# Optimization experiments

Measured on AMD Instinct MI355X. Metric: run time of the kernel, lower is better.

Reference implementation:

```python
import jax, jax.numpy as jnp
import numpy as np

B, S, D = 2, 4096, 1024
H, HD = 16, 64
CF = 0.5
K = int(S * CF)          # top_k tokens routed through the block
HIDDEN = 4 * D
EPS = 1e-5
SCALE = 1.0 / float(np.sqrt(HD))


def rmsnorm(x, w):
    return x * jax.lax.rsqrt(jnp.mean(x * x, axis=-1, keepdims=True) + EPS) * w


def rope(x, cos, sin):
    # x: [B,K,H,HD]; cos/sin: [K, HD//2]
    x1, x2 = x[..., ::2], x[..., 1::2]
    c = cos[None, :, None, :]
    s = sin[None, :, None, :]
    r1 = x1 * c - x2 * s
    r2 = x1 * s + x2 * c
    return jnp.stack([r1, r2], axis=-1).reshape(x.shape)


def block(x, mask, cos, sin, attn_norm, wq, wk, wv, wo, ffn_norm, w1, w2, w3):
    # Llama-style decoder block on the routed subset x: [B,K,D]
    b, k, _ = x.shape
    xn = rmsnorm(x, attn_norm)
    q = (xn @ wq).reshape(b, k, H, HD)
    kk = (xn @ wk).reshape(b, k, H, HD)
    v = (xn @ wv).reshape(b, k, H, HD)
    q = rope(q, cos, sin)
    kk = rope(kk, cos, sin)
    scores = jnp.einsum('bqhd,bkhd->bhqk', q, kk) * SCALE
    scores = jnp.where(mask[None, None], scores, jnp.finfo(scores.dtype).min)
    attn = jax.nn.softmax(scores, axis=-1)
    o = jnp.einsum('bhqk,bkhd->bqhd', attn, v).reshape(b, k, D)
    h = x + o @ wo
    hn = rmsnorm(h, ffn_norm)
    return h + (jax.nn.silu(hn @ w1) * (hn @ w3)) @ w2


def setup_inputs() -> dict:
    key = jax.random.key(0)
    ks = jax.random.split(key, 10)
    sc = 0.02
    inv = 1.0 / (10000.0 ** (np.arange(0, HD, 2, dtype=np.float32) / HD))
    ang = np.outer(np.arange(K, dtype=np.float32), inv)  # [K, HD//2]
    return {
        'x': jax.random.normal(ks[0], (B, S, D), jnp.float32),
        'mask': jnp.tril(jnp.ones((K, K), dtype=bool)),
        'freqs_cos': jnp.asarray(np.cos(ang)),
        'freqs_sin': jnp.asarray(np.sin(ang)),
        'w_router': jax.random.normal(ks[1], (D, 1), jnp.float32) * sc,
        'attn_norm': jnp.ones((D,), jnp.float32),
        'wq': jax.random.normal(ks[2], (D, D), jnp.float32) * sc,
        'wk': jax.random.normal(ks[3], (D, D), jnp.float32) * sc,
        'wv': jax.random.normal(ks[4], (D, D), jnp.float32) * sc,
        'wo': jax.random.normal(ks[5], (D, D), jnp.float32) * sc,
        'ffn_norm': jnp.ones((D,), jnp.float32),
        'w1': jax.random.normal(ks[6], (D, HIDDEN), jnp.float32) * sc,
        'w2': jax.random.normal(ks[7], (HIDDEN, D), jnp.float32) * sc,
        'w3': jax.random.normal(ks[8], (D, HIDDEN), jnp.float32) * sc,
    }


def reference(x, mask, freqs_cos, freqs_sin, w_router, attn_norm, wq, wk, wv, wo, ffn_norm, w1, w2, w3):
    b = x.shape[0]
    router_logits = (x @ w_router)[..., 0]            # [B,S]
    vals, idx = jax.lax.top_k(router_logits, K)       # [B,K]
    order = jnp.argsort(idx, axis=1)                  # torch.sort of token_index
    sel = jnp.take_along_axis(idx, order, axis=1)     # sorted selected positions
    token_w = jax.nn.softmax(vals, axis=1)            # softmax over topk weights
    r_weights = jnp.take_along_axis(token_w, order, axis=1)  # [B,K]
    filtered_x = jnp.take_along_axis(x, sel[:, :, None], axis=1)  # [B,K,D]
    x_out = block(filtered_x, mask, freqs_cos, freqs_sin, attn_norm,
                  wq, wk, wv, wo, ffn_norm, w1, w2, w3)
    xw_out = r_weights[:, :, None] * x_out
    # scatter_add back into the residual stream
    out = x.at[jnp.arange(b)[:, None], sel, :].add(xw_out)
    return out
```

## Files before the change

### kernel.cpp

```cpp
#include <hip/hip_runtime.h>
#include <cstdint>
#include <cstddef>

typedef unsigned short u16;
typedef __bf16 bf16x8 __attribute__((ext_vector_type(8)));
typedef short s16x4 __attribute__((ext_vector_type(4)));
typedef float f32x4 __attribute__((ext_vector_type(4)));

#define SCALE_Q_LOG2E 0.18033688011112042f

static __device__ __forceinline__ float b2f(u16 u){ return __uint_as_float(((unsigned)u)<<16); }
static __device__ __forceinline__ u16 f2b(float f){
  unsigned u = __float_as_uint(f);
  return (u16)((u + 0x7fffu + ((u>>16)&1u)) >> 16);
}
static __device__ __forceinline__ void gload_lds16(const void* g, void* l){
  auto gp = reinterpret_cast<__attribute__((address_space(1))) uint32_t*>(reinterpret_cast<uintptr_t>(g));
  auto lp = reinterpret_cast<__attribute__((address_space(3))) uint32_t*>(reinterpret_cast<uintptr_t>(l));
  __builtin_amdgcn_global_load_lds(gp, lp, 16, 0, 0);
}
static __device__ __forceinline__ f32x4 mfma16bf(s16x4 a, s16x4 b, f32x4 c){
#if __has_builtin(__builtin_amdgcn_mfma_f32_16x16x16bf16_1k)
  return __builtin_amdgcn_mfma_f32_16x16x16bf16_1k(a, b, c, 0, 0, 0);
#else
  f32x4 d = c;
  asm volatile("v_mfma_f32_16x16x16_bf16 %0, %1, %2, %0" : "+v"(d) : "v"(a), "v"(b));
  return d;
#endif
}

__global__ __launch_bounds__(256) void prep_kernel(
    const float* __restrict__ wq, const float* __restrict__ wk,
    const float* __restrict__ wv, const float* __restrict__ wo,
    const float* __restrict__ w1, const float* __restrict__ w3,
    const float* __restrict__ w2, const float* __restrict__ x,
    const float* __restrict__ wr,
    u16* __restrict__ WqkvT, u16* __restrict__ WoT,
    u16* __restrict__ W13T, u16* __restrict__ W2T,
    float* __restrict__ logits, float* __restrict__ out){
  __shared__ float tile[32][33];
  int bx = blockIdx.x;
  if (bx < 12288 || (bx >= 12288 && bx < 13312) || (bx>=13312 && bx<16384)){ }
  if (bx < 16384){
    const float* in; u16* outp; int R, C, rowmap, tcol, trow;
    if (bx < 4096){
      int wsel = bx>>10, tid = bx&1023;
      in = (wsel==0)?wq:(wsel==1)?wk:(wsel==2)?wv:wo;
      outp = (wsel<3) ? (WqkvT + (size_t)wsel*1024*1024) : WoT;
      R=1024; C=1024; rowmap=0; tcol=tid&31; trow=tid>>5;
    } else if (bx < 12288){
      int wsel=(bx-4096)>>12, tid=(bx-4096)&4095;
      in = wsel ? w3 : w1; outp = W13T; R=1024; C=4096; rowmap=1+wsel;
      tcol=tid&127; trow=tid>>7;
    } else {
      int tid = bx-12288;
      in = w2; outp = W2T; R=4096; C=1024; rowmap=0;
      tcol=tid&31; trow=tid>>5;
    }
    int t=threadIdx.x, tx=t&31, ty=t>>5;
    int c0=tcol*32, r0=trow*32;
    #pragma unroll
    for (int i=0;i<4;i++) tile[ty+i*8][tx] = in[(size_t)(r0+ty+i*8)*C + c0+tx];
    __syncthreads();
    #pragma unroll
    for (int i=0;i<4;i++){
      int c = c0+ty+i*8;
      int orow = c;
      if (rowmap==1) orow = (c>>4)*32 + (c&15);
      else if (rowmap==2) orow = (c>>4)*32 + 16 + (c&15);
      outp[(size_t)orow*R + r0+tx] = f2b(tile[tx][ty+i*8]);
    }
  } else if (bx < 18432){
    int row = (bx-16384)*4 + (threadIdx.x>>6);
    int l = threadIdx.x & 63;
    const float4* xr = (const float4*)(x + (size_t)row*1024) + l;
    const float4* wp = (const float4*)wr + l;
    float acc = 0.f;
    #pragma unroll
    for (int c=0;c<4;c++){
      float4 xv = xr[c*64];
      float4 wv = wp[c*64];
      acc += xv.x*wv.x + xv.y*wv.y + xv.z*wv.z + xv.w*wv.w;
    }
    #pragma unroll
    for (int m=1;m<64;m<<=1) acc += __shfl_xor(acc, m, 64);
    if (l==0) logits[row] = acc;
  } else {
    size_t idx = ((size_t)(bx-18432)*256 + threadIdx.x)*4;
    *(float4*)(out+idx) = *(const float4*)(x+idx);
  }
}

__global__ __launch_bounds__(256) void transpose_bf16(const u16* __restrict__ in, u16* __restrict__ out,
                                                      int R, int C){
  __shared__ u16 tile[32][33];
  size_t zoff = (size_t)blockIdx.z * R * C;
  const u16* ip = in + zoff;
  u16* op = out + zoff;
  int tx = threadIdx.x, ty = threadIdx.y;
  int c0 = blockIdx.x*32, r0 = blockIdx.y*32;
  #pragma unroll
  for (int i=0;i<4;i++) tile[ty+i*8][tx] = ip[(size_t)(r0+ty+i*8)*C + c0+tx];
  __syncthreads();
  #pragma unroll
  for (int i=0;i<4;i++) op[(size_t)(c0+ty+i*8)*R + r0+tx] = tile[tx][ty+i*8];
}

static __device__ __forceinline__ unsigned mapkey(float f){
  unsigned u = __float_as_uint(f);
  return (u & 0x80000000u) ? ~u : (u | 0x80000000u);
}
static __device__ unsigned blk_scan_excl(unsigned cnt, unsigned* swav){
  int t = threadIdx.x; int l = t&63, w = t>>6;
  unsigned v = cnt;
  #pragma unroll
  for (int off=1; off<64; off<<=1){
    unsigned n = __shfl_up(v, off, 64);
    if (l >= off) v += n;
  }
  __syncthreads();
  if (l==63) swav[w] = v;
  __syncthreads();
  if (t==0){ unsigned c=0; for (int i=0;i<16;i++){ unsigned tmp=swav[i]; swav[i]=c; c+=tmp; } }
  __syncthreads();
  return swav[w] + v - cnt;
}
__global__ __launch_bounds__(1024) void topk_kernel(const float* __restrict__ logits,
        int* __restrict__ sel, float* __restrict__ rw, int* __restrict__ inv){
  int b = blockIdx.x, t = threadIdx.x;
  int l = t&63, w = t>>6;
  __shared__ float vals[4096];
  __shared__ unsigned hist[256];
  __shared__ unsigned swav[16];
  __shared__ float fwav[16];
  __shared__ unsigned sh_prefix, sh_remaining;
  const float* lgp = logits + b*4096;
  for (int i=t;i<4096;i+=1024) vals[i]=lgp[i];
  if (t==0){ sh_prefix=0u; sh_remaining=2048u; }
  __syncthreads();
  for (int level=0; level<4; level++){
    int shift = 24 - level*8;
    if (t<256) hist[t]=0u;
    __syncthreads();
    unsigned pfx = sh_prefix;
    for (int i=t;i<4096;i+=1024){
      unsigned key = mapkey(vals[i]);
      if (level==0 || (key >> (shift+8)) == pfx)
        atomicAdd(&hist[(key>>shift)&255u], 1u);
    }
    __syncthreads();
    if (t==0){
      unsigned rem = sh_remaining, cum=0u; unsigned bsel=0u;
      for (int bin=255; bin>=0; bin--){
        unsigned hc = hist[bin];
        if (cum + hc >= rem){ bsel=(unsigned)bin; break; }
        cum += hc;
      }
      sh_remaining = rem - cum;
      sh_prefix = (pfx<<8) | bsel;
    }
    __syncthreads();
  }
  unsigned T = sh_prefix;
  unsigned req = sh_remaining;
  int i0 = t*4;
  unsigned gt_[4], eq_[4], fl_[4]; float v_[4];
  #pragma unroll
  for (int j=0;j<4;j++){
    v_[j] = vals[i0+j];
    unsigned key = mapkey(v_[j]);
    gt_[j] = key > T ? 1u:0u;
    eq_[j] = key == T ? 1u:0u;
  }
  unsigned eqbase = blk_scan_excl(eq_[0]+eq_[1]+eq_[2]+eq_[3], swav);
  unsigned er = eqbase;
  #pragma unroll
  for (int j=0;j<4;j++){ fl_[j] = gt_[j] | (eq_[j] & (er < req ? 1u:0u)); er += eq_[j]; }
  unsigned pbase = blk_scan_excl(fl_[0]+fl_[1]+fl_[2]+fl_[3], swav);
  unsigned p = pbase;
  #pragma unroll
  for (int j=0;j<4;j++){
    int i = i0+j;
    if (fl_[j]){ sel[b*2048+(int)p]=i; inv[b*4096+i]=(int)p; p++; }
    else inv[b*4096+i] = -1;
  }
  float mx = fmaxf(fmaxf(v_[0],v_[1]), fmaxf(v_[2],v_[3]));
  #pragma unroll
  for (int m=1;m<64;m<<=1) mx = fmaxf(mx, __shfl_xor(mx,m,64));
  __syncthreads();
  if (l==0) fwav[w]=mx;
  __syncthreads();
  if (t==0){ float g=fwav[0]; for(int i=1;i<16;i++) g=fmaxf(g,fwav[i]); fwav[0]=g; }
  __syncthreads();
  float gm = fwav[0];
  float zz = 0.f;
  #pragma unroll
  for (int j=0;j<4;j++) if (fl_[j]) zz += expf(v_[j]-gm);
  #pragma unroll
  for (int m=1;m<64;m<<=1) zz += __shfl_xor(zz,m,64);
  __syncthreads();
  if (l==0) fwav[w]=zz;
  __syncthreads();
  if (t==0){ float s=0.f; for(int i=0;i<16;i++) s+=fwav[i]; fwav[0]=s; }
  __syncthreads();
  float Z = fwav[0];
  unsigned p2 = pbase;
  #pragma unroll
  for (int j=0;j<4;j++) if (fl_[j]){ rw[b*2048+(int)p2] = expf(v_[j]-gm)/Z; p2++; }
}

__global__ __launch_bounds__(256) void rmsnorm_kernel(const float* __restrict__ xin,
        const float* __restrict__ gamma, const int* __restrict__ sel,
        u16* __restrict__ xn){
  int r = blockIdx.x;
  int src = r;
  if (sel) src = (r>>11)*4096 + sel[r];
  const float* row = xin + (size_t)src*1024;
  int t = threadIdx.x, l = t&63, w = t>>6;
  int d0 = t*4;
  float4 xv = *(const float4*)(row + d0);
  float ss = xv.x*xv.x + xv.y*xv.y + xv.z*xv.z + xv.w*xv.w;
  #pragma unroll
  for (int m=1;m<64;m<<=1) ss += __shfl_xor(ss,m,64);
  __shared__ float red[4];
  if (l==0) red[w]=ss;
  __syncthreads();
  float tot = red[0]+red[1]+red[2]+red[3];
  float rms = rsqrtf(tot*(1.f/1024.f) + 1e-5f);
  float4 gv = *(const float4*)(gamma + d0);
  u16 o0=f2b(xv.x*rms*gv.x), o1=f2b(xv.y*rms*gv.y), o2=f2b(xv.z*rms*gv.z), o3=f2b(xv.w*rms*gv.w);
  uint2 ov; ov.x = (unsigned)o0 | ((unsigned)o1<<16); ov.y = (unsigned)o2 | ((unsigned)o3<<16);
  *(uint2*)(xn + (size_t)r*1024 + d0) = ov;
}

template<int BK>
static __device__ __forceinline__ int swz(int row, int blk){
  if constexpr (BK==64) return blk ^ (row&7);
  else                  return blk ^ ((row>>1)&3);
}

template<int BN, int BK, typename OT>
__global__ __launch_bounds__(256,2) void gemm_bt(const u16* __restrict__ A, const u16* __restrict__ Bt,
        OT* __restrict__ C, const float* __restrict__ resid, const int* __restrict__ sel,
        int M, int N, int Kd){
  __shared__ u16 As[128*BK];
  __shared__ u16 Bs[BN*BK];
  constexpr int NF = BN/32;
  constexpr int KK = BK/32;
  int t = threadIdx.x, w = t>>6, l = t&63, lg = l>>4, ln = l&15;
  int m0 = blockIdx.y*128, n0 = blockIdx.x*BN;
  int wm = (w&1)*64, wn = (w>>1)*(BN/2);
  f32x4 acc[4][NF] = {};
  for (int k0=0; k0<Kd; k0+=BK){
    __syncthreads();
    #pragma unroll
    for (int c=0;c<128*BK*2/4096;c++){
      int off = t*16 + c*4096;
      int row = off/(BK*2), pb = (off%(BK*2))>>4;
      gload_lds16(A + (size_t)(m0+row)*Kd + k0 + swz<BK>(row,pb)*8, &As[c*2048 + w*512]);
    }
    #pragma unroll
    for (int c=0;c<BN*BK*2/4096;c++){
      int off = t*16 + c*4096;
      int row = off/(BK*2), pb = (off%(BK*2))>>4;
      gload_lds16(Bt + (size_t)(n0+row)*Kd + k0 + swz<BK>(row,pb)*8, &Bs[c*2048 + w*512]);
    }
    __syncthreads();
    #pragma unroll
    for (int kk=0;kk<KK;kk++){
      bf16x8 af[4], bfv[NF];
      #pragma unroll
      for (int i=0;i<4;i++){
        int r = wm+i*16+ln;
        af[i] = *(const bf16x8*)&As[r*BK + swz<BK>(r, kk*4+lg)*8];
      }
      #pragma unroll
      for (int i=0;i<NF;i++){
        int r = wn+i*16+ln;
        bfv[i] = *(const bf16x8*)&Bs[r*BK + swz<BK>(r, kk*4+lg)*8];
      }
      #pragma unroll
      for (int mi=0;mi<4;mi++)
        #pragma unroll
        for (int ni=0;ni<NF;ni++)
          acc[mi][ni] = __builtin_amdgcn_mfma_f32_16x16x32_bf16(af[mi], bfv[ni], acc[mi][ni], 0,0,0);
    }
  }
  #pragma unroll
  for (int mi=0;mi<4;mi++){
    #pragma unroll
    for (int ni=0;ni<NF;ni++){
      #pragma unroll
      for (int r=0;r<4;r++){
        int row = m0+wm+mi*16+lg*4+r;
        int col = n0+wn+ni*16+ln;
        float v = acc[mi][ni][r];
        if (resid){
          size_t rrow = sel ? ((size_t)(row>>11)*4096 + sel[row]) : (size_t)row;
          v += resid[rrow*N + col];
        }
        if constexpr (sizeof(OT)==2) C[(size_t)row*N + col] = f2b(v);
        else                          C[(size_t)row*N + col] = v;
      }
    }
  }
}

__global__ __launch_bounds__(256,2) void gemm_w2(const u16* __restrict__ A, const u16* __restrict__ Bt,
        const float* __restrict__ x, const float* __restrict__ hbuf,
        const int* __restrict__ sel, const float* __restrict__ rw,
        float* __restrict__ out, int Kd){
  constexpr int BN = 64, BK = 64;
  __shared__ u16 As[128*BK];
  __shared__ u16 Bs[BN*BK];
  int t = threadIdx.x, w = t>>6, l = t&63, lg = l>>4, ln = l&15;
  int m0 = blockIdx.y*128, n0 = blockIdx.x*BN;
  int wm = (w&1)*64, wn = (w>>1)*(BN/2);
  f32x4 acc[4][2] = {};
  for (int k0=0; k0<Kd; k0+=BK){
    __syncthreads();
    #pragma unroll
    for (int c=0;c<4;c++){
      int off = t*16 + c*4096;
      int row = off/(BK*2), pb = (off%(BK*2))>>4;
      gload_lds16(A + (size_t)(m0+row)*Kd + k0 + swz<BK>(row,pb)*8, &As[c*2048 + w*512]);
    }
    #pragma unroll
    for (int c=0;c<2;c++){
      int off = t*16 + c*4096;
      int row = off/(BK*2), pb = (off%(BK*2))>>4;
      gload_lds16(Bt + (size_t)(n0+row)*Kd + k0 + swz<BK>(row,pb)*8, &Bs[c*2048 + w*512]);
    }
    __syncthreads();
    #pragma unroll
    for (int kk=0;kk<2;kk++){
      bf16x8 af[4], bfv[2];
      #pragma unroll
      for (int i=0;i<4;i++){
        int r = wm+i*16+ln;
        af[i] = *(const bf16x8*)&As[r*BK + swz<BK>(r, kk*4+lg)*8];
      }
      #pragma unroll
      for (int i=0;i<2;i++){
        int r = wn+i*16+ln;
        bfv[i] = *(const bf16x8*)&Bs[r*BK + swz<BK>(r, kk*4+lg)*8];
      }
      #pragma unroll
      for (int mi=0;mi<4;mi++)
        #pragma unroll
        for (int ni=0;ni<2;ni++)
          acc[mi][ni] = __builtin_amdgcn_mfma_f32_16x16x32_bf16(af[mi], bfv[ni], acc[mi][ni], 0,0,0);
    }
  }
  #pragma unroll
  for (int mi=0;mi<4;mi++){
    int row0 = m0+wm+mi*16+lg*4;
    #pragma unroll
    for (int r=0;r<4;r++){
      int row = row0+r;
      int b = row>>11;
      size_t srow = (size_t)b*4096 + sel[row];
      float wgt = rw[row];
      #pragma unroll
      for (int ni=0;ni<2;ni++){
        int col = n0+wn+ni*16+ln;
        float y = acc[mi][ni][r];
        float v = x[srow*1024 + col] + wgt*(hbuf[(size_t)row*1024 + col] + y);
        out[srow*1024 + col] = v;
      }
    }
  }
}

__global__ __launch_bounds__(256,2) void gemm13(const u16* __restrict__ A, const u16* __restrict__ Bt,
        u16* __restrict__ g, int Kd){
  constexpr int BK = 64;
  __shared__ u16 As[128*BK];
  __shared__ u16 Bs[128*BK];
  int t = threadIdx.x, w = t>>6, l = t&63, lg = l>>4, ln = l&15;
  int m0 = blockIdx.y*128, n0 = blockIdx.x*128;
  int wm = (w&1)*64, wn = (w>>1)*64;
  f32x4 acc[4][4] = {};
  for (int k0=0; k0<Kd; k0+=BK){
    __syncthreads();
    #pragma unroll
    for (int c=0;c<4;c++){
      int off = t*16 + c*4096;
      int row = off/(BK*2), pb = (off%(BK*2))>>4;
      gload_lds16(A  + (size_t)(m0+row)*Kd + k0 + swz<BK>(row,pb)*8, &As[c*2048 + w*512]);
      gload_lds16(Bt + (size_t)(n0+row)*Kd + k0 + swz<BK>(row,pb)*8, &Bs[c*2048 + w*512]);
    }
    __syncthreads();
    #pragma unroll
    for (int kk=0;kk<2;kk++){
      bf16x8 af[4], bfv[4];
      #pragma unroll
      for (int i=0;i<4;i++){
        int ra = wm+i*16+ln, rb = wn+i*16+ln;
        af[i]  = *(const bf16x8*)&As[ra*BK + swz<BK>(ra, kk*4+lg)*8];
        bfv[i] = *(const bf16x8*)&Bs[rb*BK + swz<BK>(rb, kk*4+lg)*8];
      }
      #pragma unroll
      for (int mi=0;mi<4;mi++)
        #pragma unroll
        for (int ni=0;ni<4;ni++)
          acc[mi][ni] = __builtin_amdgcn_mfma_f32_16x16x32_bf16(af[mi], bfv[ni], acc[mi][ni], 0,0,0);
    }
  }
  int gbase = (n0+wn)>>1;
  #pragma unroll
  for (int mi=0;mi<4;mi++){
    #pragma unroll
    for (int p=0;p<2;p++){
      #pragma unroll
      for (int r=0;r<4;r++){
        int row = m0+wm+mi*16+lg*4+r;
        int col = gbase + p*16 + ln;
        float a1 = acc[mi][2*p][r], a3 = acc[mi][2*p+1][r];
        float s1 = a1 / (1.f + __expf(-a1));
        g[(size_t)row*4096 + col] = f2b(s1*a3);
      }
    }
  }
}

__global__ __launch_bounds__(256) void rope_kernel(const u16* __restrict__ QKV,
        const float* __restrict__ fcos, const float* __restrict__ fsin,
        u16* __restrict__ q_r, u16* __restrict__ k_r, u16* __restrict__ v_r){
  int row = blockIdx.x;
  int tok = row & 2047;
  int t = threadIdx.x;
  int d0 = t*4;
  int h = d0 >> 6, wd = d0 & 63, i0 = wd >> 1;
  const u16* base = QKV + (size_t)row*3072;
  size_t ob = (((size_t)(row>>11)*16 + h)*2048 + (size_t)tok)*64 + wd;
  float c0 = fcos[tok*32+i0],   s0 = fsin[tok*32+i0];
  float c1 = fcos[tok*32+i0+1], s1 = fsin[tok*32+i0+1];
  const u16* qp = base + d0;
  float x0=b2f(qp[0]), x1=b2f(qp[1]), x2=b2f(qp[2]), x3=b2f(qp[3]);
  q_r[ob]   = f2b((x0*c0-x1*s0)*SCALE_Q_LOG2E);
  q_r[ob+1] = f2b((x0*s0+x1*c0)*SCALE_Q_LOG2E);
  q_r[ob+2] = f2b((x2*c1-x3*s1)*SCALE_Q_LOG2E);
  q_r[ob+3] = f2b((x2*s1+x3*c1)*SCALE_Q_LOG2E);
  const u16* kp = base + 1024 + d0;
  x0=b2f(kp[0]); x1=b2f(kp[1]); x2=b2f(kp[2]); x3=b2f(kp[3]);
  k_r[ob]   = f2b(x0*c0-x1*s0);
  k_r[ob+1] = f2b(x0*s0+x1*c0);
  k_r[ob+2] = f2b(x2*c1-x3*s1);
  k_r[ob+3] = f2b(x2*s1+x3*c1);
  const u16* vp = base + 2048 + d0;
  v_r[ob]=vp[0]; v_r[ob+1]=vp[1]; v_r[ob+2]=vp[2]; v_r[ob+3]=vp[3];
}

static __device__ __forceinline__ void flash_tile(
    const bf16x8 (&kf)[4][2], const s16x4 (&vf)[4][4],
    bf16x8 qf0, bf16x8 qf1, int k0, int q, bool diag,
    int lg, float& mi, float& li, f32x4* oaccT){
  f32x4 sv[4];
  #pragma unroll
  for (int ni=0;ni<4;ni++){
    f32x4 z = {};
    z = __builtin_amdgcn_mfma_f32_16x16x32_bf16(kf[ni][0], qf0, z, 0,0,0);
    z = __builtin_amdgcn_mfma_f32_16x16x32_bf16(kf[ni][1], qf1, z, 0,0,0);
    sv[ni] = z;
  }
  float rm = -1e30f;
  if (diag){
    #pragma unroll
    for (int ni=0;ni<4;ni++)
      #pragma unroll
      for (int r=0;r<4;r++){
        float xs = sv[ni][r];
        if (k0+ni*16+lg*4+r > q) xs = -1e30f;
        sv[ni][r] = xs;
        rm = fmaxf(rm, xs);
      }
  } else {
    #pragma unroll
    for (int ni=0;ni<4;ni++)
      #pragma unroll
      for (int r=0;r<4;r++) rm = fmaxf(rm, sv[ni][r]);
  }
  rm = fmaxf(rm, __shfl_xor(rm, 16, 64));
  rm = fmaxf(rm, __shfl_xor(rm, 32, 64));
  float mn = fmaxf(mi, rm);
  float alpha = exp2f(mi - mn);
  float ls = 0.f;
  s16x4 pf[4];
  #pragma unroll
  for (int ni=0;ni<4;ni++){
    float p0 = exp2f(sv[ni][0]-mn);
    float p1 = exp2f(sv[ni][1]-mn);
    float p2 = exp2f(sv[ni][2]-mn);
    float p3 = exp2f(sv[ni][3]-mn);
    ls += (p0+p1)+(p2+p3);
    s16x4 pp;
    pp[0]=(short)f2b(p0); pp[1]=(short)f2b(p1); pp[2]=(short)f2b(p2); pp[3]=(short)f2b(p3);
    pf[ni]=pp;
  }
  ls += __shfl_xor(ls, 16, 64);
  ls += __shfl_xor(ls, 32, 64);
  li = li*alpha + ls;
  mi = mn;
  #pragma unroll
  for (int dt=0; dt<4; dt++){
    f32x4 oo = oaccT[dt];
    oo[0]*=alpha; oo[1]*=alpha; oo[2]*=alpha; oo[3]*=alpha;
    #pragma unroll
    for (int ni=0;ni<4;ni++)
      oo = mfma16bf(vf[dt][ni], pf[ni], oo);
    oaccT[dt] = oo;
  }
}

__global__ __launch_bounds__(256,2) void flash_kernel(const u16* __restrict__ q_r,
        const u16* __restrict__ k_r, const u16* __restrict__ v_t, u16* __restrict__ o){
  const int S = 2048;
  int pr = blockIdx.x, bh = blockIdx.y;
  int b = bh>>4, h = bh&15;
  int t = threadIdx.x, w = t>>6, l = t&63, lg = l>>4, ln = l&15;
  __shared__ u16 Ks[2][64*72];
  __shared__ u16 Vs[2][64*72];
  const u16* qb = q_r + (size_t)bh*S*64;
  const u16* kb = k_r + (size_t)bh*S*64;
  const u16* vb = v_t + (size_t)bh*64*S;
  int rr = t>>2, p16 = (t&3)*16;
  int qlo = pr, qhi = 31-pr;
  int qAr = qlo*64 + w*16 + ln;
  int qBr = qhi*64 + w*16 + ln;
  bf16x8 qA0 = *(const bf16x8*)(qb + (size_t)qAr*64 + lg*8);
  bf16x8 qA1 = *(const bf16x8*)(qb + (size_t)qAr*64 + 32 + lg*8);
  bf16x8 qB0 = *(const bf16x8*)(qb + (size_t)qBr*64 + lg*8);
  bf16x8 qB1 = *(const bf16x8*)(qb + (size_t)qBr*64 + 32 + lg*8);
  f32x4 oA[4] = {}, oB[4] = {};
  float miA=-1e30f, liA=0.f, miB=-1e30f, liB=0.f;
  {
    *(bf16x8*)&Ks[0][rr*72+p16]   = *(const bf16x8*)(kb + (size_t)rr*64 + p16);
    *(bf16x8*)&Ks[0][rr*72+p16+8] = *(const bf16x8*)(kb + (size_t)rr*64 + p16 + 8);
    *(bf16x8*)&Vs[0][rr*72+p16]   = *(const bf16x8*)(vb + (size_t)rr*S + p16);
    *(bf16x8*)&Vs[0][rr*72+p16+8] = *(const bf16x8*)(vb + (size_t)rr*S + p16 + 8);
  }
  __syncthreads();
  for (int kv=0; kv<=qhi; kv++){
    int cur = kv&1;
    int k0 = kv*64;
    bool hasnext = kv < qhi;
    bf16x8 nk0, nk1, nv0, nv1;
    if (hasnext){
      int kn = k0 + 64;
      nk0 = *(const bf16x8*)(kb + (size_t)(kn+rr)*64 + p16);
      nk1 = *(const bf16x8*)(kb + (size_t)(kn+rr)*64 + p16 + 8);
      nv0 = *(const bf16x8*)(vb + (size_t)rr*S + kn + p16);
      nv1 = *(const bf16x8*)(vb + (size_t)rr*S + kn + p16 + 8);
    }
    bf16x8 kf[4][2]; s16x4 vf[4][4];
    #pragma unroll
    for (int ni=0;ni<4;ni++){
      kf[ni][0] = *(const bf16x8*)&Ks[cur][(ni*16+ln)*72 + lg*8];
      kf[ni][1] = *(const bf16x8*)&Ks[cur][(ni*16+ln)*72 + 32 + lg*8];
    }
    #pragma unroll
    for (int dt=0;dt<4;dt++)
      #pragma unroll
      for (int ni=0;ni<4;ni++)
        vf[dt][ni] = *(const s16x4*)&Vs[cur][(dt*16+ln)*72 + ni*16 + lg*4];
    if (kv <= qlo)
      flash_tile(kf, vf, qA0, qA1, k0, qAr, kv==qlo, lg, miA, liA, oA);
    flash_tile(kf, vf, qB0, qB1, k0, qBr, kv==qhi, lg, miB, liB, oB);
    if (hasnext){
      int nb = cur^1;
      *(bf16x8*)&Ks[nb][rr*72+p16]   = nk0;
      *(bf16x8*)&Ks[nb][rr*72+p16+8] = nk1;
      *(bf16x8*)&Vs[nb][rr*72+p16]   = nv0;
      *(bf16x8*)&Vs[nb][rr*72+p16+8] = nv1;
    }
    __syncthreads();
  }
  {
    u16* ob = o + ((size_t)(b*S+qAr))*1024 + h*64 + lg*4;
    #pragma unroll
    for (int dt=0; dt<4; dt++){
      u16 a0=f2b(oA[dt][0]/liA), a1=f2b(oA[dt][1]/liA);
      u16 a2=f2b(oA[dt][2]/liA), a3=f2b(oA[dt][3]/liA);
      uint2 pv; pv.x = (unsigned)a0 | ((unsigned)a1<<16); pv.y = (unsigned)a2 | ((unsigned)a3<<16);
      *(uint2*)(ob + dt*16) = pv;
    }
  }
  {
    u16* ob = o + ((size_t)(b*S+qBr))*1024 + h*64 + lg*4;
    #pragma unroll
    for (int dt=0; dt<4; dt++){
      u16 a0=f2b(oB[dt][0]/liB), a1=f2b(oB[dt][1]/liB);
      u16 a2=f2b(oB[dt][2]/liB), a3=f2b(oB[dt][3]/liB);
      uint2 pv; pv.x = (unsigned)a0 | ((unsigned)a1<<16); pv.y = (unsigned)a2 | ((unsigned)a3<<16);
      *(uint2*)(ob + dt*16) = pv;
    }
  }
}

extern "C" void kernel_launch(void* const* d_in, const int* in_sizes, int n_in,
                              void* d_out, int out_size, void* d_ws, size_t ws_size,
                              hipStream_t stream) {
  (void)in_sizes; (void)n_in; (void)out_size; (void)ws_size;
  const float* x     = (const float*)d_in[0];
  const float* fcos  = (const float*)d_in[2];
  const float* fsin  = (const float*)d_in[3];
  const float* wr    = (const float*)d_in[4];
  const float* anorm = (const float*)d_in[5];
  const float* wq    = (const float*)d_in[6];
  const float* wk    = (const float*)d_in[7];
  const float* wv    = (const float*)d_in[8];
  const float* wo    = (const float*)d_in[9];
  const float* fnorm = (const float*)d_in[10];
  const float* w1    = (const float*)d_in[11];
  const float* w2    = (const float*)d_in[12];
  const float* w3    = (const float*)d_in[13];
  float* out = (float*)d_out;

  char* W = (char*)d_ws;
  const size_t MB = 1024*1024;
  u16* WqkvT = (u16*)(W + 0);
  u16* WoT   = (u16*)(W + 6*MB);
  u16* W13T  = (u16*)(W + 8*MB);
  u16* W2T   = (u16*)(W + 24*MB);
  u16* xn    = (u16*)(W + 32*MB);
  u16* QKV   = (u16*)(W + 40*MB);
  u16* q_r   = (u16*)(W + 64*MB);
  u16* k_r   = (u16*)(W + 72*MB);
  u16* v_r   = (u16*)(W + 80*MB);
  u16* v_t   = (u16*)(W + 88*MB);
  u16* attno = (u16*)(W + 96*MB);
  float* hbuf= (float*)(W + 104*MB);
  u16* hn    = (u16*)(W + 120*MB);
  u16* g     = (u16*)(W + 128*MB);
  float* logits = (float*)(W + 160*MB);
  int*   sel    = (int*)(W + 160*MB + 64*1024);
  float* rw     = (float*)(W + 160*MB + 96*1024);
  int*   inv    = (int*)(W + 160*MB + 128*1024);
  (void)inv;

  prep_kernel<<<26624, 256, 0, stream>>>(wq, wk, wv, wo, w1, w3, w2, x, wr,
                                         WqkvT, WoT, W13T, W2T, logits, out);
  topk_kernel<<<2, 1024, 0, stream>>>(logits, sel, rw, (int*)(W + 160*MB + 128*1024));
  rmsnorm_kernel<<<4096, 256, 0, stream>>>(x, anorm, sel, xn);
  gemm_bt<128,64,u16><<<dim3(24,32), 256, 0, stream>>>(xn, WqkvT, QKV, nullptr, nullptr, 4096, 3072, 1024);
  rope_kernel<<<4096, 256, 0, stream>>>(QKV, fcos, fsin, q_r, k_r, v_r);
  transpose_bf16<<<dim3(2,64,32), dim3(32,8), 0, stream>>>(v_r, v_t, 2048, 64);
  flash_kernel<<<dim3(16,32), 256, 0, stream>>>(q_r, k_r, v_t, attno);
  gemm_bt<64,64,float><<<dim3(16,32), 256, 0, stream>>>(attno, WoT, hbuf, x, sel, 4096, 1024, 1024);
  rmsnorm_kernel<<<4096, 256, 0, stream>>>(hbuf, fnorm, nullptr, hn);
  gemm13<<<dim3(64,32), 256, 0, stream>>>(hn, W13T, g, 1024);
  gemm_w2<<<dim3(16,32), 256, 0, stream>>>(g, W2T, x, hbuf, sel, rw, out, 4096);
}
```

Before: 491.6 us.

## Run FFN GEMMs in FP8 with scaled weights and FP8 activations

Converts W1/W3/W2 weights to FP8 with a fixed scale and quantizes the FFN normalized activations and gated hidden to FP8. The FFN GEMMs then use the fp8 MFMA instruction with BK=128. This halves the operand bytes and doubles MFMA throughput for the largest GEMMs. The copy of x into out moves from a prep kernel branch to an async device memcpy. FP8 quantization adds accuracy risk that tolerance checks may flag.

```diff
diff --git a/kernel.cpp b/kernel.cpp
--- a/kernel.cpp
+++ b/kernel.cpp
@@ -3,16 +3,22 @@
 #include <cstddef>
 
 typedef unsigned short u16;
+typedef unsigned char u8;
 typedef __bf16 bf16x8 __attribute__((ext_vector_type(8)));
 typedef short s16x4 __attribute__((ext_vector_type(4)));
 typedef float f32x4 __attribute__((ext_vector_type(4)));
 
 #define SCALE_Q_LOG2E 0.18033688011112042f
+#define W_SCALE 64.0f
+#define INV_W_SCALE 0.015625f
 
 static __device__ __forceinline__ float b2f(u16 u){ return __uint_as_float(((unsigned)u)<<16); }
 static __device__ __forceinline__ u16 f2b(float f){
   unsigned u = __float_as_uint(f);
   return (u16)((u + 0x7fffu + ((u>>16)&1u)) >> 16);
+}
+static __device__ __forceinline__ u8 f2fp8(float f){
+  return (u8)(__builtin_amdgcn_cvt_pk_fp8_f32(f, f, 0, false) & 0xff);
 }
 static __device__ __forceinline__ void gload_lds16(const void* g, void* l){
   auto gp = reinterpret_cast<__attribute__((address_space(1))) uint32_t*>(reinterpret_cast<uintptr_t>(g));
@@ -36,43 +42,47 @@
     const float* __restrict__ w2, const float* __restrict__ x,
     const float* __restrict__ wr,
     u16* __restrict__ WqkvT, u16* __restrict__ WoT,
-    u16* __restrict__ W13T, u16* __restrict__ W2T,
-    float* __restrict__ logits, float* __restrict__ out){
+    u8* __restrict__ W13T, u8* __restrict__ W2T,
+    float* __restrict__ logits){
   __shared__ float tile[32][33];
   int bx = blockIdx.x;
-  if (bx < 12288 || (bx >= 12288 && bx < 13312) || (bx>=13312 && bx<16384)){ }
-  if (bx < 16384){
-    const float* in; u16* outp; int R, C, rowmap, tcol, trow;
-    if (bx < 4096){
-      int wsel = bx>>10, tid = bx&1023;
-      in = (wsel==0)?wq:(wsel==1)?wk:(wsel==2)?wv:wo;
-      outp = (wsel<3) ? (WqkvT + (size_t)wsel*1024*1024) : WoT;
-      R=1024; C=1024; rowmap=0; tcol=tid&31; trow=tid>>5;
-    } else if (bx < 12288){
-      int wsel=(bx-4096)>>12, tid=(bx-4096)&4095;
-      in = wsel ? w3 : w1; outp = W13T; R=1024; C=4096; rowmap=1+wsel;
-      tcol=tid&127; trow=tid>>7;
-    } else {
-      int tid = bx-12288;
-      in = w2; outp = W2T; R=4096; C=1024; rowmap=0;
-      tcol=tid&31; trow=tid>>5;
-    }
-    int t=threadIdx.x, tx=t&31, ty=t>>5;
-    int c0=tcol*32, r0=trow*32;
-    #pragma unroll
-    for (int i=0;i<4;i++) tile[ty+i*8][tx] = in[(size_t)(r0+ty+i*8)*C + c0+tx];
+  int t=threadIdx.x, tx=t&31, ty=t>>5;
+  if (bx < 4096){
+    int wsel = bx>>10, tid = bx&1023;
+    const float* in = (wsel==0)?wq:(wsel==1)?wk:(wsel==2)?wv:wo;
+    u16* outp = (wsel<3) ? (WqkvT + (size_t)wsel*1024*1024) : WoT;
+    int c0=(tid&31)*32, r0=(tid>>5)*32;
+    #pragma unroll
+    for (int i=0;i<4;i++) tile[ty+i*8][tx] = in[(size_t)(r0+ty+i*8)*1024 + c0+tx];
+    __syncthreads();
+    #pragma unroll
+    for (int i=0;i<4;i++)
+      outp[(size_t)(c0+ty+i*8)*1024 + r0+tx] = f2b(tile[tx][ty+i*8]);
+  } else if (bx < 12288){
+    int wsel=(bx-4096)>>12, tid=(bx-4096)&4095;
+    const float* in = wsel ? w3 : w1;
+    int c0=(tid&127)*32, r0=(tid>>7)*32;
+    #pragma unroll
+    for (int i=0;i<4;i++) tile[ty+i*8][tx] = in[(size_t)(r0+ty+i*8)*4096 + c0+tx];
     __syncthreads();
     #pragma unroll
     for (int i=0;i<4;i++){
       int c = c0+ty+i*8;
-      int orow = c;
-      if (rowmap==1) orow = (c>>4)*32 + (c&15);
-      else if (rowmap==2) orow = (c>>4)*32 + 16 + (c&15);
-      outp[(size_t)orow*R + r0+tx] = f2b(tile[tx][ty+i*8]);
-    }
-  } else if (bx < 18432){
-    int row = (bx-16384)*4 + (threadIdx.x>>6);
-    int l = threadIdx.x & 63;
+      int orow = (c>>4)*32 + (wsel?16:0) + (c&15);
+      W13T[(size_t)orow*1024 + r0+tx] = f2fp8(tile[tx][ty+i*8]*W_SCALE);
+    }
+  } else if (bx < 16384){
+    int tid = bx-12288;
+    int c0=(tid&31)*32, r0=(tid>>5)*32;
+    #pragma unroll
+    for (int i=0;i<4;i++) tile[ty+i*8][tx] = w2[(size_t)(r0+ty+i*8)*1024 + c0+tx];
+    __syncthreads();
+    #pragma unroll
+    for (int i=0;i<4;i++)
+      W2T[(size_t)(c0+ty+i*8)*4096 + r0+tx] = f2fp8(tile[tx][ty+i*8]*W_SCALE);
+  } else {
+    int row = (bx-16384)*4 + (t>>6);
+    int l = t & 63;
     const float4* xr = (const float4*)(x + (size_t)row*1024) + l;
     const float4* wp = (const float4*)wr + l;
     float acc = 0.f;
@@ -85,9 +95,6 @@
     #pragma unroll
     for (int m=1;m<64;m<<=1) acc += __shfl_xor(acc, m, 64);
     if (l==0) logits[row] = acc;
-  } else {
-    size_t idx = ((size_t)(bx-18432)*256 + threadIdx.x)*4;
-    *(float4*)(out+idx) = *(const float4*)(x+idx);
   }
 }
 
@@ -209,9 +216,10 @@
   for (int j=0;j<4;j++) if (fl_[j]){ rw[b*2048+(int)p2] = expf(v_[j]-gm)/Z; p2++; }
 }
 
+template<typename OT>
 __global__ __launch_bounds__(256) void rmsnorm_kernel(const float* __restrict__ xin,
         const float* __restrict__ gamma, const int* __restrict__ sel,
-        u16* __restrict__ xn){
+        OT* __restrict__ xn){
   int r = blockIdx.x;
   int src = r;
   if (sel) src = (r>>11)*4096 + sel[r];
@@ -228,15 +236,23 @@
   float tot = red[0]+red[1]+red[2]+red[3];
   float rms = rsqrtf(tot*(1.f/1024.f) + 1e-5f);
   float4 gv = *(const float4*)(gamma + d0);
-  u16 o0=f2b(xv.x*rms*gv.x), o1=f2b(xv.y*rms*gv.y), o2=f2b(xv.z*rms*gv.z), o3=f2b(xv.w*rms*gv.w);
-  uint2 ov; ov.x = (unsigned)o0 | ((unsigned)o1<<16); ov.y = (unsigned)o2 | ((unsigned)o3<<16);
-  *(uint2*)(xn + (size_t)r*1024 + d0) = ov;
-}
-
-template<int BK>
+  float v0=xv.x*rms*gv.x, v1=xv.y*rms*gv.y, v2=xv.z*rms*gv.z, v3=xv.w*rms*gv.w;
+  if constexpr (sizeof(OT)==2){
+    uint2 ov; ov.x = (unsigned)f2b(v0) | ((unsigned)f2b(v1)<<16);
+    ov.y = (unsigned)f2b(v2) | ((unsigned)f2b(v3)<<16);
+    *(uint2*)(xn + (size_t)r*1024 + d0) = ov;
+  } else {
+    unsigned pw = (unsigned)__builtin_amdgcn_cvt_pk_fp8_f32(v0, v1, 0, false);
+    pw = (unsigned)__builtin_amdgcn_cvt_pk_fp8_f32(v2, v3, (int)pw, true);
+    *(unsigned*)((u8*)xn + (size_t)r*1024 + d0) = pw;
+  }
+}
+
+template<int NB>
 static __device__ __forceinline__ int swz(int row, int blk){
-  if constexpr (BK==64) return blk ^ (row&7);
-  else                  return blk ^ ((row>>1)&3);
+  if constexpr (NB==8) return blk ^ (row&7);
+  else if constexpr (NB==4) return blk ^ ((row>>1)&3);
+  else return blk ^ ((row>>1)&3);
 }
 
 template<int BN, int BK, typename OT>
@@ -247,6 +263,7 @@
   __shared__ u16 Bs[BN*BK];
   constexpr int NF = BN/32;
   constexpr int KK = BK/32;
+  constexpr int NB = BK/8;
   int t = threadIdx.x, w = t>>6, l = t&63, lg = l>>4, ln = l&15;
   int m0 = blockIdx.y*128, n0 = blockIdx.x*BN;
   int wm = (w&1)*64, wn = (w>>1)*(BN/2);
@@ -257,13 +274,13 @@
     for (int c=0;c<128*BK*2/4096;c++){
       int off = t*16 + c*4096;
       int row = off/(BK*2), pb = (off%(BK*2))>>4;
-      gload_lds16(A + (size_t)(m0+row)*Kd + k0 + swz<BK>(row,pb)*8, &As[c*2048 + w*512]);
+      gload_lds16(A + (size_t)(m0+row)*Kd + k0 + swz<NB>(row,pb)*8, &As[c*2048 + w*512]);
     }
     #pragma unroll
     for (int c=0;c<BN*BK*2/4096;c++){
       int off = t*16 + c*4096;
       int row = off/(BK*2), pb = (off%(BK*2))>>4;
-      gload_lds16(Bt + (size_t)(n0+row)*Kd + k0 + swz<BK>(row,pb)*8, &Bs[c*2048 + w*512]);
+      gload_lds16(Bt + (size_t)(n0+row)*Kd + k0 + swz<NB>(row,pb)*8, &Bs[c*2048 + w*512]);
     }
     __syncthreads();
     #pragma unroll
@@ -272,12 +289,12 @@
       #pragma unroll
       for (int i=0;i<4;i++){
         int r = wm+i*16+ln;
-        af[i] = *(const bf16x8*)&As[r*BK + swz<BK>(r, kk*4+lg)*8];
+        af[i] = *(const bf16x8*)&As[r*BK + swz<NB>(r, kk*4+lg)*8];
       }
       #pragma unroll
       for (int i=0;i<NF;i++){
         int r = wn+i*16+ln;
-        bfv[i] = *(const bf16x8*)&Bs[r*BK + swz<BK>(r, kk*4+lg)*8];
+        bfv[i] = *(const bf16x8*)&Bs[r*BK + swz<NB>(r, kk*4+lg)*8];
       }
       #pragma unroll
       for (int mi=0;mi<4;mi++)
@@ -306,13 +323,66 @@
   }
 }
 
-__global__ __launch_bounds__(256,2) void gemm_w2(const u16* __restrict__ A, const u16* __restrict__ Bt,
+__global__ __launch_bounds__(256,2) void gemm13(const u8* __restrict__ A, const u8* __restrict__ Bt,
+        u8* __restrict__ g, int Kd){
+  constexpr int BK = 128;
+  __shared__ u8 As[128*BK];
+  __shared__ u8 Bs[128*BK];
+  int t = threadIdx.x, w = t>>6, l = t&63, lg = l>>4, ln = l&15;
+  int m0 = blockIdx.y*128, n0 = blockIdx.x*128;
+  int wm = (w&1)*64, wn = (w>>1)*64;
+  f32x4 acc[4][4] = {};
+  for (int k0=0; k0<Kd; k0+=BK){
+    __syncthreads();
+    #pragma unroll
+    for (int c=0;c<4;c++){
+      int off = t*16 + c*4096;
+      int row = off>>7, pb = (off&127)>>4;
+      gload_lds16(A  + (size_t)(m0+row)*Kd + k0 + ((pb^(row&7))<<4), &As[c*4096 + w*1024]);
+      gload_lds16(Bt + (size_t)(n0+row)*Kd + k0 + ((pb^(row&7))<<4), &Bs[c*4096 + w*1024]);
+    }
+    __syncthreads();
+    #pragma unroll
+    for (int kk=0;kk<4;kk++){
+      long long af[4], bfv[4];
+      #pragma unroll
+      for (int i=0;i<4;i++){
+        int ra = wm+i*16+ln, rb = wn+i*16+ln;
+        int g0 = kk*2 + (lg>>1), ho = (lg&1)*8;
+        af[i]  = *(const long long*)&As[ra*BK + ((g0^(ra&7))<<4) + ho];
+        bfv[i] = *(const long long*)&Bs[rb*BK + ((g0^(rb&7))<<4) + ho];
+      }
+      #pragma unroll
+      for (int mi=0;mi<4;mi++)
+        #pragma unroll
+        for (int ni=0;ni<4;ni++)
+          acc[mi][ni] = __builtin_amdgcn_mfma_f32_16x16x32_fp8_fp8(af[mi], bfv[ni], acc[mi][ni], 0,0,0);
+    }
+  }
+  int gbase = (n0+wn)>>1;
+  #pragma unroll
+  for (int mi=0;mi<4;mi++){
+    #pragma unroll
+    for (int p=0;p<2;p++){
+      #pragma unroll
+      for (int r=0;r<4;r++){
+        int row = m0+wm+mi*16+lg*4+r;
+        int col = gbase + p*16 + ln;
+        float a1 = acc[mi][2*p][r]*INV_W_SCALE, a3 = acc[mi][2*p+1][r]*INV_W_SCALE;
+        float s1 = a1 / (1.f + __expf(-a1));
+        g[(size_t)row*4096 + col] = f2fp8(s1*a3);
+      }
+    }
+  }
+}
+
+__global__ __launch_bounds__(256,2) void gemm_w2(const u8* __restrict__ A, const u8* __restrict__ Bt,
         const float* __restrict__ x, const float* __restrict__ hbuf,
         const int* __restrict__ sel, const float* __restrict__ rw,
         float* __restrict__ out, int Kd){
-  constexpr int BN = 64, BK = 64;
-  __shared__ u16 As[128*BK];
-  __shared__ u16 Bs[BN*BK];
+  constexpr int BN = 64, BK = 128;
+  __shared__ u8 As[128*BK];
+  __shared__ u8 Bs[BN*BK];
   int t = threadIdx.x, w = t>>6, l = t&63, lg = l>>4, ln = l&15;
   int m0 = blockIdx.y*128, n0 = blockIdx.x*BN;
   int wm = (w&1)*64, wn = (w>>1)*(BN/2);
@@ -322,34 +392,35 @@
     #pragma unroll
     for (int c=0;c<4;c++){
       int off = t*16 + c*4096;
-      int row = off/(BK*2), pb = (off%(BK*2))>>4;
-      gload_lds16(A + (size_t)(m0+row)*Kd + k0 + swz<BK>(row,pb)*8, &As[c*2048 + w*512]);
+      int row = off>>7, pb = (off&127)>>4;
+      gload_lds16(A + (size_t)(m0+row)*Kd + k0 + ((pb^(row&7))<<4), &As[c*4096 + w*1024]);
     }
     #pragma unroll
     for (int c=0;c<2;c++){
       int off = t*16 + c*4096;
-      int row = off/(BK*2), pb = (off%(BK*2))>>4;
-      gload_lds16(Bt + (size_t)(n0+row)*Kd + k0 + swz<BK>(row,pb)*8, &Bs[c*2048 + w*512]);
-    }
-    __syncthreads();
-    #pragma unroll
-    for (int kk=0;kk<2;kk++){
-      bf16x8 af[4], bfv[2];
+      int row = off>>7, pb = (off&127)>>4;
+      gload_lds16(Bt + (size_t)(n0+row)*Kd + k0 + ((pb^(row&7))<<4), &Bs[c*4096 + w*1024]);
+    }
+    __syncthreads();
+    #pragma unroll
+    for (int kk=0;kk<4;kk++){
+      long long af[4], bfv[2];
+      int g0 = kk*2 + (lg>>1), ho = (lg&1)*8;
       #pragma unroll
       for (int i=0;i<4;i++){
         int r = wm+i*16+ln;
-        af[i] = *(const bf16x8*)&As[r*BK + swz<BK>(r, kk*4+lg)*8];
+        af[i] = *(const long long*)&As[r*BK + ((g0^(r&7))<<4) + ho];
       }
       #pragma unroll
       for (int i=0;i<2;i++){
         int r = wn+i*16+ln;
-        bfv[i] = *(const bf16x8*)&Bs[r*BK + swz<BK>(r, kk*4+lg)*8];
+        bfv[i] = *(const long long*)&Bs[r*BK + ((g0^(r&7))<<4) + ho];
       }
       #pragma unroll
       for (int mi=0;mi<4;mi++)
         #pragma unroll
         for (int ni=0;ni<2;ni++)
-          acc[mi][ni] = __builtin_amdgcn_mfma_f32_16x16x32_bf16(af[mi], bfv[ni], acc[mi][ni], 0,0,0);
+          acc[mi][ni] = __builtin_amdgcn_mfma_f32_16x16x32_fp8_fp8(af[mi], bfv[ni], acc[mi][ni], 0,0,0);
     }
   }
   #pragma unroll
@@ -364,61 +435,8 @@
       #pragma unroll
       for (int ni=0;ni<2;ni++){
         int col = n0+wn+ni*16+ln;
-        float y = acc[mi][ni][r];
-        float v = x[srow*1024 + col] + wgt*(hbuf[(size_t)row*1024 + col] + y);
-        out[srow*1024 + col] = v;
-      }
-    }
-  }
-}
-
-__global__ __launch_bounds__(256,2) void gemm13(const u16* __restrict__ A, const u16* __restrict__ Bt,
-        u16* __restrict__ g, int Kd){
-  constexpr int BK = 64;
-  __shared__ u16 As[128*BK];
-  __shared__ u16 Bs[128*BK];
-  int t = threadIdx.x, w = t>>6, l = t&63, lg = l>>4, ln = l&15;
-  int m0 = blockIdx.y*128, n0 = blockIdx.x*128;
-  int wm = (w&1)*64, wn = (w>>1)*64;
-  f32x4 acc[4][4] = {};
-  for (int k0=0; k0<Kd; k0+=BK){
-    __syncthreads();
-    #pragma unroll
-    for (int c=0;c<4;c++){
-      int off = t*16 + c*4096;
-      int row = off/(BK*2), pb = (off%(BK*2))>>4;
-      gload_lds16(A  + (size_t)(m0+row)*Kd + k0 + swz<BK>(row,pb)*8, &As[c*2048 + w*512]);
-      gload_lds16(Bt + (size_t)(n0+row)*Kd + k0 + swz<BK>(row,pb)*8, &Bs[c*2048 + w*512]);
-    }
-    __syncthreads();
-    #pragma unroll
-    for (int kk=0;kk<2;kk++){
-      bf16x8 af[4], bfv[4];
-      #pragma unroll
-      for (int i=0;i<4;i++){
-        int ra = wm+i*16+ln, rb = wn+i*16+ln;
-        af[i]  = *(const bf16x8*)&As[ra*BK + swz<BK>(ra, kk*4+lg)*8];
-        bfv[i] = *(const bf16x8*)&Bs[rb*BK + swz<BK>(rb, kk*4+lg)*8];
-      }
-      #pragma unroll
-      for (int mi=0;mi<4;mi++)
-        #pragma unroll
-        for (int ni=0;ni<4;ni++)
-          acc[mi][ni] = __builtin_amdgcn_mfma_f32_16x16x32_bf16(af[mi], bfv[ni], acc[mi][ni], 0,0,0);
-    }
-  }
-  int gbase = (n0+wn)>>1;
-  #pragma unroll
-  for (int mi=0;mi<4;mi++){
-    #pragma unroll
-    for (int p=0;p<2;p++){
-      #pragma unroll
-      for (int r=0;r<4;r++){
-        int row = m0+wm+mi*16+lg*4+r;
-        int col = gbase + p*16 + ln;
-        float a1 = acc[mi][2*p][r], a3 = acc[mi][2*p+1][r];
-        float s1 = a1 / (1.f + __expf(-a1));
-        g[(size_t)row*4096 + col] = f2b(s1*a3);
+        float y = acc[mi][ni][r]*INV_W_SCALE;
+        out[srow*1024 + col] = x[srow*1024 + col] + wgt*(hbuf[(size_t)row*1024 + col] + y);
       }
     }
   }
@@ -621,34 +639,34 @@
   const size_t MB = 1024*1024;
   u16* WqkvT = (u16*)(W + 0);
   u16* WoT   = (u16*)(W + 6*MB);
-  u16* W13T  = (u16*)(W + 8*MB);
-  u16* W2T   = (u16*)(W + 24*MB);
-  u16* xn    = (u16*)(W + 32*MB);
-  u16* QKV   = (u16*)(W + 40*MB);
-  u16* q_r   = (u16*)(W + 64*MB);
-  u16* k_r   = (u16*)(W + 72*MB);
-  u16* v_r   = (u16*)(W + 80*MB);
-  u16* v_t   = (u16*)(W + 88*MB);
-  u16* attno = (u16*)(W + 96*MB);
-  float* hbuf= (float*)(W + 104*MB);
-  u16* hn    = (u16*)(W + 120*MB);
-  u16* g     = (u16*)(W + 128*MB);
-  float* logits = (float*)(W + 160*MB);
-  int*   sel    = (int*)(W + 160*MB + 64*1024);
-  float* rw     = (float*)(W + 160*MB + 96*1024);
-  int*   inv    = (int*)(W + 160*MB + 128*1024);
-  (void)inv;
-
-  prep_kernel<<<26624, 256, 0, stream>>>(wq, wk, wv, wo, w1, w3, w2, x, wr,
-                                         WqkvT, WoT, W13T, W2T, logits, out);
-  topk_kernel<<<2, 1024, 0, stream>>>(logits, sel, rw, (int*)(W + 160*MB + 128*1024));
-  rmsnorm_kernel<<<4096, 256, 0, stream>>>(x, anorm, sel, xn);
+  u8*  W13T  = (u8*)(W + 8*MB);
+  u8*  W2T   = (u8*)(W + 16*MB);
+  u16* xn    = (u16*)(W + 20*MB);
+  u16* QKV   = (u16*)(W + 28*MB);
+  u16* q_r   = (u16*)(W + 52*MB);
+  u16* k_r   = (u16*)(W + 60*MB);
+  u16* v_r   = (u16*)(W + 68*MB);
+  u16* v_t   = (u16*)(W + 76*MB);
+  u16* attno = (u16*)(W + 84*MB);
+  float* hbuf= (float*)(W + 92*MB);
+  u8*  hn8   = (u8*)(W + 108*MB);
+  u8*  g     = (u8*)(W + 112*MB);
+  float* logits = (float*)(W + 128*MB);
+  int*   sel    = (int*)(W + 128*MB + 64*1024);
+  float* rw     = (float*)(W + 128*MB + 96*1024);
+  int*   inv    = (int*)(W + 128*MB + 128*1024);
+
+  hipMemcpyAsync(out, x, (size_t)8192*1024*4, hipMemcpyDeviceToDevice, stream);
+  prep_kernel<<<18432, 256, 0, stream>>>(wq, wk, wv, wo, w1, w3, w2, x, wr,
+                                         WqkvT, WoT, W13T, W2T, logits);
+  topk_kernel<<<2, 1024, 0, stream>>>(logits, sel, rw, inv);
+  rmsnorm_kernel<u16><<<4096, 256, 0, stream>>>(x, anorm, sel, xn);
   gemm_bt<128,64,u16><<<dim3(24,32), 256, 0, stream>>>(xn, WqkvT, QKV, nullptr, nullptr, 4096, 3072, 1024);
   rope_kernel<<<4096, 256, 0, stream>>>(QKV, fcos, fsin, q_r, k_r, v_r);
   transpose_bf16<<<dim3(2,64,32), dim3(32,8), 0, stream>>>(v_r, v_t, 2048, 64);
   flash_kernel<<<dim3(16,32), 256, 0, stream>>>(q_r, k_r, v_t, attno);
   gemm_bt<64,64,float><<<dim3(16,32), 256, 0, stream>>>(attno, WoT, hbuf, x, sel, 4096, 1024, 1024);
-  rmsnorm_kernel<<<4096, 256, 0, stream>>>(hbuf, fnorm, nullptr, hn);
-  gemm13<<<dim3(64,32), 256, 0, stream>>>(hn, W13T, g, 1024);
+  rmsnorm_kernel<u8><<<4096, 256, 0, stream>>>(hbuf, fnorm, nullptr, hn8);
+  gemm13<<<dim3(64,32), 256, 0, stream>>>(hn8, W13T, g, 1024);
   gemm_w2<<<dim3(16,32), 256, 0, stream>>>(g, W2T, x, hbuf, sel, rw, out, 4096);
 }
```

Result: faster. 436.0 us (-11.3%).
